# Kernel tuning notes

Hardware: AMD Instinct MI355X
Metric: run time of the kernel (lower is better)

## Reference

```python
import jax, jax.numpy as jnp
import numpy as np

EPS = 1e-7  # K.epsilon()
ROUTINGS = 3


def squash(v, axis=-1):
    s2 = jnp.sum(jnp.square(v), axis=axis, keepdims=True)
    scale = s2 / (1.0 + s2) / jnp.sqrt(s2 + EPS)
    return scale * v


def setup_inputs() -> dict:
    key = jax.random.key(0)
    k1, k2 = jax.random.split(key)
    B, I, D_IN = 64, 2048, 16
    J, D_OUT = 32, 32
    inputs = jax.random.normal(k1, (B, I, D_IN), dtype=jnp.float32)
    W = jax.random.normal(k2, (J, I, D_OUT, D_IN), dtype=jnp.float32) * 0.05
    return {"inputs": inputs, "W": W}


def reference(inputs, W):
    # u_hat[b,j,i,e] = sum_d inputs[b,i,d] * W[j,i,e,d]
    u_hat = jnp.einsum('bid,jied->bjie', inputs, W)  # [B, J, I, D_out]
    B, J, I, _ = u_hat.shape
    b = jnp.zeros((B, J, I), dtype=u_hat.dtype)
    outputs = None
    for r in range(ROUTINGS):
        c = jax.nn.softmax(b, axis=1)                 # softmax over output capsules J
        s = jnp.einsum('bji,bjie->bje', c, u_hat)     # weighted sum over input capsules
        outputs = squash(s)                           # [B, J, D_out]
        if r < ROUTINGS - 1:
            b = b + jnp.einsum('bje,bjie->bji', outputs, u_hat)
    return outputs
```

## Files before the change

### kernel.cpp

```cpp
#include <hip/hip_runtime.h>
#include <hip/hip_bf16.h>

#define NB 64
#define NI 2048
#define ND 16
#define NJ 32
#define NE 32
#define NIP (NI/2)
#define NKC 64
#define NSL NKC

typedef __attribute__((ext_vector_type(8))) short bfrag;
typedef __attribute__((ext_vector_type(4))) float f32x4;

__device__ inline unsigned pk2bf(float a, float b) {
    __hip_bfloat162 h = __float22bfloat162_rn(make_float2(a, b));
    return *reinterpret_cast<unsigned*>(&h);
}

template <int N>
__device__ inline float rot16_add(float v) {
    int r = __builtin_amdgcn_mov_dpp(__float_as_int(v), 0x120 + N, 0xf, 0xf, false);
    return v + __int_as_float(r);
}

__device__ inline unsigned scale_pair(unsigned u, float cc) {
    float f0 = __uint_as_float(u << 16);
    float f1 = __uint_as_float(u & 0xffff0000u);
    return pk2bf(f0 * cc, f1 * cc);
}

__global__ __launch_bounds__(256) void convxT_k(const float* __restrict__ x,
                                                short* __restrict__ xT)
{
    const int T = blockIdx.x * 256 + threadIdx.x;
    const int i = T >> 6, b = T & 63;
    const float4* src = reinterpret_cast<const float4*>(
        x + ((size_t)b * NI + i) * ND);
    float4 a0 = src[0], a1 = src[1], a2 = src[2], a3 = src[3];
    bfrag lo, hi;
    unsigned* lu = reinterpret_cast<unsigned*>(&lo);
    unsigned* hu = reinterpret_cast<unsigned*>(&hi);
    lu[0] = pk2bf(a0.x, a0.y); lu[1] = pk2bf(a0.z, a0.w);
    lu[2] = pk2bf(a1.x, a1.y); lu[3] = pk2bf(a1.z, a1.w);
    hu[0] = pk2bf(a2.x, a2.y); hu[1] = pk2bf(a2.z, a2.w);
    hu[2] = pk2bf(a3.x, a3.y); hu[3] = pk2bf(a3.z, a3.w);
    short* dst = xT + ((size_t)i * NB + b) * ND;
    *reinterpret_cast<bfrag*>(dst)     = lo;
    *reinterpret_cast<bfrag*>(dst + 8) = hi;
}

__global__ __launch_bounds__(512) void fwd_k(
    const short* __restrict__ xT,
    const short* __restrict__ Wb,
    const float* __restrict__ Oacc,
    float* __restrict__ part)
{
    const int l    = blockIdx.x;
    const int grp  = l >> 5;
    const int bb   = (l >> 3) & 3;
    const int ic   = grp * 8 + (l & 7);
    const int b0   = bb * 16;
    const int i0   = ic * 16;
    const int t    = threadIdx.x;
    const int wv   = t >> 6;
    const int ln   = t & 63;
    const int m    = ln & 15;
    const int quad = ln >> 4;

    __shared__ float lsm[16][NJ][16];

    float O0[4][4], O1[4][4];
#pragma unroll
    for (int jj = 0; jj < 4; ++jj) {
        const int j = wv * 4 + jj;
#pragma unroll
        for (int r = 0; r < 4; ++r) {
            const int b = b0 + quad * 4 + r;
            O0[jj][r] = Oacc[((size_t)b * NJ + j) * NE + m];
            O1[jj][r] = Oacc[((size_t)b * NJ + j) * NE + 16 + m];
        }
    }

    const int  bA  = b0 + m;
    const bool act = quad < 2;
    const int  d0  = quad * 8;

    for (int il = 0; il < 16; ++il) {
        const int i = i0 + il;
        const int ip = i >> 1, isel = i & 1;
        bfrag av = (bfrag)0;
        if (act) {
            av = *reinterpret_cast<const bfrag*>(
                xT + ((size_t)i * NB + bA) * ND + d0);
        }
#pragma unroll
        for (int jj = 0; jj < 4; ++jj) {
            const int j = wv * 4 + jj;
            bfrag bv0 = (bfrag)0, bv1 = (bfrag)0;
            if (act) {
                const short* wp = Wb + (((size_t)j * NIP + ip) * NE + m) * 32
                                     + isel * 16 + d0;
                bv0 = *reinterpret_cast<const bfrag*>(wp);
                bv1 = *reinterpret_cast<const bfrag*>(wp + 16 * 32);
            }
            f32x4 z = {0.f, 0.f, 0.f, 0.f};
            f32x4 U0 = __builtin_amdgcn_mfma_f32_16x16x32_bf16(av, bv0, z, 0, 0, 0);
            f32x4 U1 = __builtin_amdgcn_mfma_f32_16x16x32_bf16(av, bv1, z, 0, 0, 0);

            float v4[4];
#pragma unroll
            for (int r = 0; r < 4; ++r) {
                float v = fmaf(U0[r], O0[jj][r], U1[r] * O1[jj][r]);
                v = rot16_add<1>(v);
                v = rot16_add<2>(v);
                v = rot16_add<4>(v);
                v = rot16_add<8>(v);
                v4[r] = v;
            }
            if (m == 0) {
                *reinterpret_cast<float4*>(&lsm[il][j][quad * 4]) =
                    make_float4(v4[0], v4[1], v4[2], v4[3]);
            }
        }
    }
    __syncthreads();

    if (t < 256) {
        const int il = t >> 4, b = t & 15;
        float mx = -1e30f;
#pragma unroll
        for (int jx = 0; jx < NJ; ++jx) mx = fmaxf(mx, lsm[il][jx][b]);
        float sum = 0.f;
#pragma unroll
        for (int jx = 0; jx < NJ; ++jx) {
            const float e = __expf(lsm[il][jx][b] - mx);
            lsm[il][jx][b] = e;
            sum += e;
        }
        const float inv = 1.0f / sum;
#pragma unroll
        for (int jx = 0; jx < NJ; ++jx) lsm[il][jx][b] *= inv;
    }
    __syncthreads();

    f32x4 acc0[4] = {{0.f,0.f,0.f,0.f},{0.f,0.f,0.f,0.f},
                     {0.f,0.f,0.f,0.f},{0.f,0.f,0.f,0.f}};
    f32x4 acc1[4] = {{0.f,0.f,0.f,0.f},{0.f,0.f,0.f,0.f},
                     {0.f,0.f,0.f,0.f},{0.f,0.f,0.f,0.f}};
    for (int il = 0; il < 16; ++il) {
        const int i = i0 + il;
        const int ip = i >> 1, isel = i & 1;
        uint4 xr = {0u, 0u, 0u, 0u};
        if (act) {
            xr = *reinterpret_cast<const uint4*>(
                xT + ((size_t)i * NB + bA) * ND + d0);
        }
#pragma unroll
        for (int jj = 0; jj < 4; ++jj) {
            const int j = wv * 4 + jj;
            const float cv = lsm[il][j][m];
            bfrag av2;
            unsigned* au = reinterpret_cast<unsigned*>(&av2);
            au[0] = scale_pair(xr.x, cv);
            au[1] = scale_pair(xr.y, cv);
            au[2] = scale_pair(xr.z, cv);
            au[3] = scale_pair(xr.w, cv);
            bfrag bv0 = (bfrag)0, bv1 = (bfrag)0;
            if (act) {
                const short* wp = Wb + (((size_t)j * NIP + ip) * NE + m) * 32
                                     + isel * 16 + d0;
                bv0 = *reinterpret_cast<const bfrag*>(wp);
                bv1 = *reinterpret_cast<const bfrag*>(wp + 16 * 32);
            }
            acc0[jj] = __builtin_amdgcn_mfma_f32_16x16x32_bf16(av2, bv0, acc0[jj], 0, 0, 0);
            acc1[jj] = __builtin_amdgcn_mfma_f32_16x16x32_bf16(av2, bv1, acc1[jj], 0, 0, 0);
        }
    }

    float* base = part + ((size_t)(bb * 128 + ic) * NJ) * 512;
#pragma unroll
    for (int jj = 0; jj < 4; ++jj) {
        const int j = wv * 4 + jj;
#pragma unroll
        for (int r = 0; r < 4; ++r) {
            float* p = base + (size_t)j * 512 + (quad * 4 + r) * 32 + m;
            p[0]  = acc0[jj][r];
            p[16] = acc1[jj][r];
        }
    }
}

__global__ __launch_bounds__(512) void rs2_k(
    const float* __restrict__ part,
    float* __restrict__ Oacc,
    float* __restrict__ out,
    int mode)
{
    const int G2 = blockIdx.x * 512 + threadIdx.x;
    const int row = G2 >> 2;
    const int q   = G2 & 3;
    const int e = row & 31, j = (row >> 5) & 31, b = row >> 10;
    const int bb = b >> 4, bl = b & 15;

    const float* p = part + ((size_t)(bb * 128 + q * 32) * NJ + j) * 512
                          + bl * 32 + e;
    float sum = 0.f;
#pragma unroll 8
    for (int s = 0; s < 32; ++s)
        sum += p[(size_t)s * NJ * 512];

    __shared__ float lds[512];
    lds[threadIdx.x] = sum;
    __syncthreads();

    if (threadIdx.x < 128) {
        const int t4 = threadIdx.x * 4;
        const float s = lds[t4] + lds[t4 + 1] + lds[t4 + 2] + lds[t4 + 3];
        const int row2 = blockIdx.x * 128 + threadIdx.x;
        const int e2 = row2 & 31, j2 = (row2 >> 5) & 31, b2 = row2 >> 10;
        float qq = s * s;
        qq += __shfl_xor(qq, 1);
        qq += __shfl_xor(qq, 2);
        qq += __shfl_xor(qq, 4);
        qq += __shfl_xor(qq, 8);
        qq += __shfl_xor(qq, 16);
        const float scale = qq / ((1.0f + qq) * sqrtf(qq + 1e-7f));
        const float o = scale * s;
        const size_t off = ((size_t)b2 * NJ + j2) * NE + e2;
        if (mode == 2) out[off] = o;
        else           Oacc[off] += o;
    }
}


#define WS_LOAD(P, itv)                                                        \
    {   const int ip_ = ip0 + (itv);                                           \
        const int ia_ = ip_ * 2 + isel;                                        \
        {                                                                      \
            const float* wp_ = Wsrc + (((size_t)j * NI + ia_) * NE + m) * ND + d0; \
            P##w0 = *reinterpret_cast<const float4*>(wp_);                     \
            P##w1 = *reinterpret_cast<const float4*>(wp_ + 4);                 \
            P##w2 = *reinterpret_cast<const float4*>(wp_ + 16 * ND);           \
            P##w3 = *reinterpret_cast<const float4*>(wp_ + 16 * ND + 4);       \
        }                                                                      \
        const short* xp_ = xT + ((size_t)ia_ * NB + m) * ND + d0;              \
        P##x0 = *reinterpret_cast<const uint4*>(xp_);                          \
        P##x1 = *reinterpret_cast<const uint4*>(xp_ + 16 * ND);                \
        P##x2 = *reinterpret_cast<const uint4*>(xp_ + 32 * ND);                \
        P##x3 = *reinterpret_cast<const uint4*>(xp_ + 48 * ND);                \
    }

#define WS_MT(XV, A0, A1)                                                      \
    {   const float cc_ = 1.0f / NJ;                                           \
        bfrag av_;                                                             \
        unsigned* au_ = reinterpret_cast<unsigned*>(&av_);                     \
        au_[0] = scale_pair((XV).x, cc_); au_[1] = scale_pair((XV).y, cc_);    \
        au_[2] = scale_pair((XV).z, cc_); au_[3] = scale_pair((XV).w, cc_);    \
        A0 = __builtin_amdgcn_mfma_f32_16x16x32_bf16(av_, bv0_, A0, 0, 0, 0);  \
        A1 = __builtin_amdgcn_mfma_f32_16x16x32_bf16(av_, bv1_, A1, 0, 0, 0);  \
    }

#define WS_COMPUTE(P, itv)                                                     \
    {   bfrag bv0_, bv1_;                                                      \
        {                                                                      \
            unsigned* b0_ = reinterpret_cast<unsigned*>(&bv0_);                \
            unsigned* b1_ = reinterpret_cast<unsigned*>(&bv1_);                \
            b0_[0] = pk2bf(P##w0.x, P##w0.y); b0_[1] = pk2bf(P##w0.z, P##w0.w);\
            b0_[2] = pk2bf(P##w1.x, P##w1.y); b0_[3] = pk2bf(P##w1.z, P##w1.w);\
            b1_[0] = pk2bf(P##w2.x, P##w2.y); b1_[1] = pk2bf(P##w2.z, P##w2.w);\
            b1_[2] = pk2bf(P##w3.x, P##w3.y); b1_[3] = pk2bf(P##w3.z, P##w3.w);\
            short* wd_ = Wb + (((size_t)j * NIP + (ip0 + (itv))) * NE + m) * 32 + quad * 8; \
            *reinterpret_cast<bfrag*>(wd_)       = bv0_;                       \
            *reinterpret_cast<bfrag*>(wd_ + 512) = bv1_;                       \
        }                                                                      \
        WS_MT(P##x0, a00, a01)                                                 \
        WS_MT(P##x1, a10, a11)                                                 \
        WS_MT(P##x2, a20, a21)                                                 \
        WS_MT(P##x3, a30, a31)                                                 \
    }

__global__ __launch_bounds__(128) void wsum_k(
    const float* __restrict__ Wsrc,
    const short* __restrict__ xT,
    short* __restrict__ Wb,
    float* __restrict__ partial)
{
    const int l    = blockIdx.x;
    const int x    = l & 7;
    const int r    = l >> 3;
    const int j    = r & 31;
    const int kc   = x * 8 + (r >> 5);
    const int t    = threadIdx.x;
    const int wv   = t >> 6;
    const int ln   = t & 63;
    const int m    = ln & 15;
    const int quad = ln >> 4;
    const int isel = quad >> 1;
    const int d0   = (quad & 1) * 8;
    const int ip0  = kc * 16 + wv * 8;

    __shared__ float red[2][2048];

    f32x4 a00 = {0.f,0.f,0.f,0.f}, a01 = {0.f,0.f,0.f,0.f};
    f32x4 a10 = {0.f,0.f,0.f,0.f}, a11 = {0.f,0.f,0.f,0.f};
    f32x4 a20 = {0.f,0.f,0.f,0.f}, a21 = {0.f,0.f,0.f,0.f};
    f32x4 a30 = {0.f,0.f,0.f,0.f}, a31 = {0.f,0.f,0.f,0.f};

    float4 Aw0, Aw1, Aw2, Aw3, Bw0, Bw1, Bw2, Bw3;
    uint4  Ax0, Ax1, Ax2, Ax3, Bx0, Bx1, Bx2, Bx3;

    WS_LOAD(A, 0)
    WS_LOAD(B, 1)
    WS_COMPUTE(A, 0)
    WS_LOAD(A, 2)
    WS_COMPUTE(B, 1)
    WS_LOAD(B, 3)
    WS_COMPUTE(A, 2)
    WS_LOAD(A, 4)
    WS_COMPUTE(B, 3)
    WS_LOAD(B, 5)
    WS_COMPUTE(A, 4)
    WS_LOAD(A, 6)
    WS_COMPUTE(B, 5)
    WS_LOAD(B, 7)
    WS_COMPUTE(A, 6)
    WS_COMPUTE(B, 7)

    float* rb = &red[wv][0];
    *reinterpret_cast<f32x4*>(rb + 0 * 256 + ln * 4) = a00;
    *reinterpret_cast<f32x4*>(rb + 1 * 256 + ln * 4) = a01;
    *reinterpret_cast<f32x4*>(rb + 2 * 256 + ln * 4) = a10;
    *reinterpret_cast<f32x4*>(rb + 3 * 256 + ln * 4) = a11;
    *reinterpret_cast<f32x4*>(rb + 4 * 256 + ln * 4) = a20;
    *reinterpret_cast<f32x4*>(rb + 5 * 256 + ln * 4) = a21;
    *reinterpret_cast<f32x4*>(rb + 6 * 256 + ln * 4) = a30;
    *reinterpret_cast<f32x4*>(rb + 7 * 256 + ln * 4) = a31;
    __syncthreads();

    float* pb = partial + ((size_t)kc * NJ + j) * 2048;
#pragma unroll
    for (int k = 0; k < 4; ++k) {
        const int g = k * 512 + t * 4;
        f32x4 s = *reinterpret_cast<const f32x4*>(&red[0][g]);
        s += *reinterpret_cast<const f32x4*>(&red[1][g]);
        *reinterpret_cast<f32x4*>(pb + g) = s;
    }
}

__global__ __launch_bounds__(512) void rs_k(
    const float* __restrict__ partial,
    float* __restrict__ Oacc,
    float* __restrict__ out,
    int mode)
{
    const int G    = blockIdx.x * 512 + threadIdx.x;
    const int j    = G >> 11;
    const int g    = G & 2047;
    const int group = g >> 8;
    const int mt   = group >> 1;
    const int nt   = group & 1;
    const int lnn  = (g >> 2) & 63;
    const int m    = lnn & 15;
    const int quad = lnn >> 4;
    const int r    = g & 3;
    const int b    = mt * 16 + quad * 4 + r;
    const int e    = nt * 16 + m;

    float sum = 0.f;
#pragma unroll 8
    for (int sl = 0; sl < NSL; ++sl)
        sum += partial[((size_t)sl * NJ + j) * 2048 + g];

    __shared__ float lds[512];
    const int row = quad * 4 + r;
    lds[row * 32 + e] = sum;
    __syncthreads();
    const float* rp = &lds[row * 32];
    float p = 0.f;
#pragma unroll
    for (int ee = 0; ee < 32; ++ee) p = fmaf(rp[ee], rp[ee], p);

    const float scale = p / ((1.0f + p) * sqrtf(p + 1e-7f));
    const float o = scale * sum;
    const size_t off = ((size_t)b * NJ + j) * NE + e;
    if (mode == 2)      out[off]  = o;
    else if (mode == 1) Oacc[off] += o;
    else                Oacc[off] = o;
}

extern "C" void kernel_launch(void* const* d_in, const int* in_sizes, int n_in,
                              void* d_out, int out_size, void* d_ws, size_t ws_size,
                              hipStream_t stream)
{
    (void)in_sizes; (void)n_in; (void)out_size; (void)ws_size;
    const float* x = (const float*)d_in[0];
    const float* W = (const float*)d_in[1];
    float* out = (float*)d_out;

    float* Oacc = (float*)d_ws;
    float* part = Oacc + NB * NJ * NE;
    short* Wb   = (short*)(part + (size_t)512 * NJ * 512);
    short* xT   = Wb + (size_t)NJ * NIP * NE * 32;

    convxT_k<<<(NI * NB) / 256, 256, 0, stream>>>(x, xT);

    wsum_k<<<NJ * NKC, 128, 0, stream>>>(W, xT, Wb, part);
    rs_k<<<65536 / 512, 512, 0, stream>>>(part, Oacc, out, 0);

    fwd_k<<<512, 512, 0, stream>>>(xT, Wb, Oacc, part);
    rs2_k<<<262144 / 512, 512, 0, stream>>>(part, Oacc, out, 1);

    fwd_k<<<512, 512, 0, stream>>>(xT, Wb, Oacc, part);
    rs2_k<<<262144 / 512, 512, 0, stream>>>(part, Oacc, out, 2);
}
```

Measured before the change: 359.0 us.

## Re-layout routing partial sums for contiguous vectorized reduction in rs2_k

```diff
diff --git a/kernel.cpp b/kernel.cpp
--- a/kernel.cpp
+++ b/kernel.cpp
@@ -178,15 +178,15 @@
         }
     }
 
-    float* base = part + ((size_t)(bb * 128 + ic) * NJ) * 512;
 #pragma unroll
     for (int jj = 0; jj < 4; ++jj) {
         const int j = wv * 4 + jj;
 #pragma unroll
         for (int r = 0; r < 4; ++r) {
-            float* p = base + (size_t)j * 512 + (quad * 4 + r) * 32 + m;
-            p[0]  = acc0[jj][r];
-            p[16] = acc1[jj][r];
+            const int bg = b0 + quad * 4 + r;
+            float* p = part + (((size_t)(bg * NJ + j) * 128) + ic) * 32;
+            p[m]      = acc0[jj][r];
+            p[m + 16] = acc1[jj][r];
         }
     }
 }
@@ -197,39 +197,39 @@
     float* __restrict__ out,
     int mode)
 {
-    const int G2 = blockIdx.x * 512 + threadIdx.x;
-    const int row = G2 >> 2;
-    const int q   = G2 & 3;
-    const int e = row & 31, j = (row >> 5) & 31, b = row >> 10;
-    const int bb = b >> 4, bl = b & 15;
-
-    const float* p = part + ((size_t)(bb * 128 + q * 32) * NJ + j) * 512
-                          + bl * 32 + e;
-    float sum = 0.f;
-#pragma unroll 8
-    for (int s = 0; s < 32; ++s)
-        sum += p[(size_t)s * NJ * 512];
-
-    __shared__ float lds[512];
-    lds[threadIdx.x] = sum;
-    __syncthreads();
-
-    if (threadIdx.x < 128) {
-        const int t4 = threadIdx.x * 4;
-        const float s = lds[t4] + lds[t4 + 1] + lds[t4 + 2] + lds[t4 + 3];
-        const int row2 = blockIdx.x * 128 + threadIdx.x;
-        const int e2 = row2 & 31, j2 = (row2 >> 5) & 31, b2 = row2 >> 10;
-        float qq = s * s;
-        qq += __shfl_xor(qq, 1);
-        qq += __shfl_xor(qq, 2);
-        qq += __shfl_xor(qq, 4);
-        qq += __shfl_xor(qq, 8);
-        qq += __shfl_xor(qq, 16);
-        const float scale = qq / ((1.0f + qq) * sqrtf(qq + 1e-7f));
-        const float o = scale * s;
-        const size_t off = ((size_t)b2 * NJ + j2) * NE + e2;
-        if (mode == 2) out[off] = o;
-        else           Oacc[off] += o;
+    const int gt = blockIdx.x * 512 + threadIdx.x;
+    const int w  = gt >> 6;
+    const int ln = gt & 63;
+
+    const float* p = part + (size_t)w * 4096;
+    f32x4 acc = {0.f, 0.f, 0.f, 0.f};
+#pragma unroll
+    for (int k = 0; k < 16; ++k) {
+        const f32x4 v = *reinterpret_cast<const f32x4*>(p + k * 256 + ln * 4);
+        acc += v;
+    }
+#pragma unroll
+    for (int i = 0; i < 4; ++i) {
+        acc[i] += __shfl_xor(acc[i], 8);
+        acc[i] += __shfl_xor(acc[i], 16);
+        acc[i] += __shfl_xor(acc[i], 32);
+    }
+    float q = acc[0]*acc[0] + acc[1]*acc[1] + acc[2]*acc[2] + acc[3]*acc[3];
+    q += __shfl_xor(q, 1);
+    q += __shfl_xor(q, 2);
+    q += __shfl_xor(q, 4);
+
+    const float scale = q / ((1.0f + q) * sqrtf(q + 1e-7f));
+    if (ln < 8) {
+        float* op = (mode == 2 ? out : Oacc) + (size_t)w * NE + ln * 4;
+        f32x4 o;
+        o[0] = scale * acc[0]; o[1] = scale * acc[1];
+        o[2] = scale * acc[2]; o[3] = scale * acc[3];
+        if (mode == 1) {
+            const f32x4 prev = *reinterpret_cast<const f32x4*>(op);
+            o += prev;
+        }
+        *reinterpret_cast<f32x4*>(op) = o;
     }
 }
 
@@ -400,7 +400,7 @@
 
     float* Oacc = (float*)d_ws;
     float* part = Oacc + NB * NJ * NE;
-    short* Wb   = (short*)(part + (size_t)512 * NJ * 512);
+    short* Wb   = (short*)(part + (size_t)NB * NJ * 128 * 32);
     short* xT   = Wb + (size_t)NJ * NIP * NE * 32;
 
     convxT_k<<<(NI * NB) / 256, 256, 0, stream>>>(x, xT);
@@ -409,8 +409,8 @@
     rs_k<<<65536 / 512, 512, 0, stream>>>(part, Oacc, out, 0);
 
     fwd_k<<<512, 512, 0, stream>>>(xT, Wb, Oacc, part);
-    rs2_k<<<262144 / 512, 512, 0, stream>>>(part, Oacc, out, 1);
+    rs2_k<<<256, 512, 0, stream>>>(part, Oacc, out, 1);
 
     fwd_k<<<512, 512, 0, stream>>>(xT, Wb, Oacc, part);
-    rs2_k<<<262144 / 512, 512, 0, stream>>>(part, Oacc, out, 2);
-}
+    rs2_k<<<256, 512, 0, stream>>>(part, Oacc, out, 2);
+}
```

Measured after the change: 358.1 us. Within noise of the previous version (-0.3%).
